# Kernel tuning notes

Hardware: AMD Instinct MI355X
Metric: run time of the kernel (lower is better)

The kernel has to match this reference:

```python
import jax, jax.numpy as jnp
import numpy as np

C_M, C_Z, C_H = 256, 128, 32
S, N = 128, 384
EPS = 1e-5


def setup_inputs() -> dict:
    key = jax.random.key(0)
    ks = jax.random.split(key, 8)
    sc = 1.0 / np.sqrt(C_M)
    return {
        "msa": jax.random.normal(ks[0], (S, N, C_M), dtype=jnp.float32),
        "ln_g": jnp.ones((C_M,), dtype=jnp.float32),
        "ln_b": jnp.zeros((C_M,), dtype=jnp.float32),
        "Wl": jax.random.uniform(ks[1], (C_M, C_H), jnp.float32, -sc, sc),
        "bl": jax.random.uniform(ks[2], (C_H,), jnp.float32, -sc, sc),
        "Wr": jax.random.uniform(ks[3], (C_M, C_H), jnp.float32, -sc, sc),
        "br": jax.random.uniform(ks[4], (C_H,), jnp.float32, -sc, sc),
        "Wo": jax.random.uniform(ks[5], (C_H * C_H, C_Z), jnp.float32, -1.0 / C_H, 1.0 / C_H),
        "bo": jax.random.uniform(ks[6], (C_Z,), jnp.float32, -1.0 / C_H, 1.0 / C_H),
    }


def _layernorm(x, g, b):
    mu = jnp.mean(x, axis=-1, keepdims=True)
    var = jnp.mean(jnp.square(x - mu), axis=-1, keepdims=True)
    return (x - mu) * jax.lax.rsqrt(var + EPS) * g + b


def reference(msa, ln_g, ln_b, Wl, bl, Wr, br, Wo, bo):
    s = msa.shape[0]
    m = _layernorm(msa, ln_g, ln_b)          # [s, n, c_m]
    left = m @ Wl + bl                        # [s, n, c_h]
    right = m @ Wr + br                       # [s, n, c_h]
    outer = jnp.einsum('sic,sjd->ijcd', left, right) / s  # [n, n, c_h, c_h]
    outer = outer.reshape(outer.shape[0], outer.shape[1], -1)
    return outer @ Wo + bo                    # [n, n, c_z]
```

## Files before the change

kernel.cpp:

```cpp
#include <hip/hip_runtime.h>
#include <hip/hip_bf16.h>

#define CM 256
#define CZ 128
#define CH 32
#define SS 128
#define NN 384

typedef short bf16x8 __attribute__((ext_vector_type(8)));
typedef float f32x4 __attribute__((ext_vector_type(4)));
typedef unsigned short us4 __attribute__((ext_vector_type(4)));
typedef unsigned short us8 __attribute__((ext_vector_type(8)));

__device__ __forceinline__ unsigned short f2bf(float f) {
    __hip_bfloat16 h = __float2bfloat16(f);
    return __builtin_bit_cast(unsigned short, h);
}

__global__ __launch_bounds__(256) void k0_transpose(
    const float* __restrict__ Wo, const float* __restrict__ Wl, const float* __restrict__ Wr,
    unsigned short* __restrict__ WoF, unsigned short* __restrict__ WT) {
    int n = blockIdx.x;
    int base = n * 1024;
#pragma unroll
    for (int u = 0; u < 4; u++) {
        int w   = base + u * 256 + threadIdx.x;
        int e   = w & 7;
        int l   = (w >> 3) & 63;
        int zb  = (w >> 9) & 7;
        int cch = w >> 12;
        WoF[w] = f2bf(Wo[(size_t)(cch * 32 + (l >> 4) * 8 + e) * CZ + zb * 16 + (l & 15)]);
    }
    int k = threadIdx.x;
    if (n < 32) {
        WT[n * CM + k] = f2bf(Wl[(size_t)k * CH + n]);
    } else if (n < 64) {
        WT[32 * CM + (n - 32) * CM + k] = f2bf(Wr[(size_t)k * CH + (n - 32)]);
    }
}

__global__ __launch_bounds__(256, 2) void k1_ln_proj(
    const float* __restrict__ msa, const float* __restrict__ g, const float* __restrict__ bta,
    const unsigned short* __restrict__ WT, const float* __restrict__ bl, const float* __restrict__ br,
    unsigned short* __restrict__ Lt, unsigned short* __restrict__ Rt)
{
    __shared__ unsigned short A_lds[64 * 264];
    __shared__ unsigned short B_lds[64 * 264];

    const int i    = blockIdx.x;
    const int sh   = blockIdx.y;
    const int t    = threadIdx.x;
    const int wv   = t >> 6;
    const int lane = t & 63;
    const int lr   = lane & 15, lg = lane >> 4;

    const float4 gv = ((const float4*)g)[lane];
    const float4 bv = ((const float4*)bta)[lane];
#pragma unroll 4
    for (int r = 0; r < 16; r++) {
        int sl = wv * 16 + r;
        int s  = sh * 64 + sl;
        float4 v = ((const float4*)(msa + ((size_t)s * NN + i) * CM))[lane];
        float sum = v.x + v.y + v.z + v.w;
        float sq  = v.x * v.x + v.y * v.y + v.z * v.z + v.w * v.w;
#pragma unroll
        for (int off = 32; off >= 1; off >>= 1) {
            sum += __shfl_xor(sum, off, 64);
            sq  += __shfl_xor(sq, off, 64);
        }
        float mu = sum * (1.f / CM);
        float rs = rsqrtf(sq * (1.f / CM) - mu * mu + 1e-5f);
        us4 pk;
        pk[0] = f2bf((v.x - mu) * rs * gv.x + bv.x);
        pk[1] = f2bf((v.y - mu) * rs * gv.y + bv.y);
        pk[2] = f2bf((v.z - mu) * rs * gv.z + bv.z);
        pk[3] = f2bf((v.w - mu) * rs * gv.w + bv.w);
        *(us4*)&A_lds[sl * 264 + lane * 4] = pk;
    }
#pragma unroll
    for (int u = 0; u < 8; u++) {
        int id = u * 256 + t;
        *(us8*)&B_lds[(id >> 5) * 264 + (id & 31) * 8] = *(const us8*)&WT[id * 8];
    }
    __syncthreads();

    const int m0 = (wv >> 1) * 32;
    const int n0 = (wv & 1) * 32;
    f32x4 acc[2][2];
#pragma unroll
    for (int a = 0; a < 2; a++)
#pragma unroll
        for (int b = 0; b < 2; b++) acc[a][b] = (f32x4){0.f, 0.f, 0.f, 0.f};

#pragma unroll
    for (int ks = 0; ks < 8; ks++) {
        int ko = ks * 32 + lg * 8;
        bf16x8 a0 = *(const bf16x8*)&A_lds[(m0 + lr) * 264 + ko];
        bf16x8 a1 = *(const bf16x8*)&A_lds[(m0 + 16 + lr) * 264 + ko];
        bf16x8 b0 = *(const bf16x8*)&B_lds[(n0 + lr) * 264 + ko];
        bf16x8 b1 = *(const bf16x8*)&B_lds[(n0 + 16 + lr) * 264 + ko];
        acc[0][0] = __builtin_amdgcn_mfma_f32_16x16x32_bf16(a0, b0, acc[0][0], 0, 0, 0);
        acc[0][1] = __builtin_amdgcn_mfma_f32_16x16x32_bf16(a0, b1, acc[0][1], 0, 0, 0);
        acc[1][0] = __builtin_amdgcn_mfma_f32_16x16x32_bf16(a1, b0, acc[1][0], 0, 0, 0);
        acc[1][1] = __builtin_amdgcn_mfma_f32_16x16x32_bf16(a1, b1, acc[1][1], 0, 0, 0);
    }

    const bool isL = (n0 == 0);
    const float scale = isL ? 0.0078125f : 1.f;
#pragma unroll
    for (int mt = 0; mt < 2; mt++)
#pragma unroll
        for (int nt = 0; nt < 2; nt++) {
            int ch = (n0 + nt * 16 + lr) & 31;
            float bias = isL ? bl[ch] : br[ch];
            us4 pk;
#pragma unroll
            for (int rg = 0; rg < 4; rg++)
                pk[rg] = f2bf((acc[mt][nt][rg] + bias) * scale);
            unsigned short* dst = (isL ? Lt : Rt) + (size_t)(i * CH + ch) * SS
                                  + sh * 64 + m0 + mt * 16 + lg * 4;
            *(us4*)dst = pk;
        }
}

#define TI 8
#define TJ 8
#define P1_B_OFF 69632
#define OH1_OFF  65536
#define K2_LDS   139264

__global__ __launch_bounds__(512, 2) void k2_fused(
    const unsigned short* __restrict__ Lt, const unsigned short* __restrict__ Rt,
    const unsigned short* __restrict__ WoF, const float* __restrict__ bo,
    float* __restrict__ out)
{
    extern __shared__ char smem[];
    unsigned short* A = (unsigned short*)(smem);
    unsigned short* B = (unsigned short*)(smem + P1_B_OFF);

    const int i0 = blockIdx.x * TI;
    const int j0 = blockIdx.y * TJ;
    const int t  = threadIdx.x;
    const int wv = t >> 6, lane = t & 63;
    const int lr = lane & 15, lg = lane >> 4;

    const unsigned short* gA = Lt + (size_t)i0 * CH * SS;
    const unsigned short* gB = Rt + (size_t)j0 * CH * SS;
#pragma unroll
    for (int it = 0; it < 8; it++) {
        int c  = it * 512 + t;
        int rw = c >> 4, kc = c & 15;
        *(us8*)(A + rw * 136 + kc * 8) = *(const us8*)(gA + rw * 128 + kc * 8);
        *(us8*)(B + rw * 136 + kc * 8) = *(const us8*)(gB + rw * 128 + kc * 8);
    }
    __syncthreads();

    const int m0  = (wv >> 2) * 128;
    const int n0w = (wv & 3) * 64;

    f32x4 accE[4][4], accO[4][4];
#pragma unroll
    for (int a = 0; a < 4; a++)
#pragma unroll
        for (int b = 0; b < 4; b++) {
            accE[a][b] = (f32x4){0.f, 0.f, 0.f, 0.f};
            accO[a][b] = (f32x4){0.f, 0.f, 0.f, 0.f};
        }

#pragma unroll
    for (int ks = 0; ks < 4; ks++) {
        int ko = ks * 32 + lg * 8;
        bf16x8 af[8], bfr[4];
#pragma unroll
        for (int mt = 0; mt < 8; mt++) af[mt]  = *(const bf16x8*)(A + (m0 + mt * 16 + lr) * 136 + ko);
#pragma unroll
        for (int nt = 0; nt < 4; nt++) bfr[nt] = *(const bf16x8*)(B + (n0w + nt * 16 + lr) * 136 + ko);
#pragma unroll
        for (int mt = 0; mt < 8; mt++)
#pragma unroll
            for (int nt = 0; nt < 4; nt++) {
                if (mt & 1)
                    accO[mt >> 1][nt] = __builtin_amdgcn_mfma_f32_16x16x32_bf16(bfr[nt], af[mt], accO[mt >> 1][nt], 0, 0, 0);
                else
                    accE[mt >> 1][nt] = __builtin_amdgcn_mfma_f32_16x16x32_bf16(bfr[nt], af[mt], accE[mt >> 1][nt], 0, 0, 0);
            }
    }
    __syncthreads();

    const int zsl = wv & 1, ksl = wv >> 1;

    bf16x8 wcur[4], wnxt[4];
#pragma unroll
    for (int bi = 0; bi < 4; bi++)
        wcur[bi] = *(const bf16x8*)&WoF[(((size_t)ksl * 8 + zsl * 4 + bi) * 64 + lane) * 8];

    {
        unsigned short* Oh0 = (unsigned short*)smem;
        unsigned short* Oh1 = (unsigned short*)(smem + OH1_OFF);
#pragma unroll
        for (int mh = 0; mh < 4; mh++) {
            int iiw  = (wv >> 2) * 4 + mh;
            int rowH = iiw * 16 + lr;
            int okey = (rowH ^ (rowH >> 4)) & 7;
#pragma unroll
            for (int nt = 0; nt < 4; nt++) {
                int colBase = n0w + nt * 16 + lg * 4;
                int chk = (colBase >> 3) ^ okey;
                int off = rowH * 256 + chk * 8 + (lg & 1) * 4;
                us4 pkE, pkO;
#pragma unroll
                for (int rg = 0; rg < 4; rg++) {
                    pkE[rg] = f2bf(accE[mh][nt][rg]);
                    pkO[rg] = f2bf(accO[mh][nt][rg]);
                }
                *(us4*)&Oh0[off] = pkE;
                *(us4*)&Oh1[off] = pkO;
            }
        }
    }
    __syncthreads();

    f32x4 acc2[4][4];
#pragma unroll
    for (int a = 0; a < 4; a++)
#pragma unroll
        for (int b = 0; b < 4; b++) acc2[a][b] = (f32x4){0.f, 0.f, 0.f, 0.f};

#pragma unroll
    for (int c = 0; c < 8; c++) {
        if (c < 7) {
            int cchn = (c + 1) * 4 + ksl;
#pragma unroll
            for (int bi = 0; bi < 4; bi++)
                wnxt[bi] = *(const bf16x8*)&WoF[(((size_t)cchn * 8 + zsl * 4 + bi) * 64 + lane) * 8];
        }

        const int cch = c * 4 + ksl;
        const int hh  = cch >> 4;
        const int cH  = cch & 15;
        const unsigned short* OhX = (const unsigned short*)(smem + (hh ? OH1_OFF : 0));

        bf16x8 af2[4];
#pragma unroll
        for (int ai = 0; ai < 4; ai++) {
            int rowH = (ai * 2 + ((lane >> 3) & 1)) * 16 + cH;
            int okey = (rowH ^ (rowH >> 4)) & 7;
            int chk  = (((lane & 7) * 4 + lg) ^ okey);
            af2[ai] = *(const bf16x8*)&OhX[rowH * 256 + chk * 8];
        }
#pragma unroll
        for (int ai = 0; ai < 4; ai++)
#pragma unroll
            for (int bi = 0; bi < 4; bi++)
                acc2[ai][bi] = __builtin_amdgcn_mfma_f32_16x16x32_bf16(af2[ai], wcur[bi], acc2[ai][bi], 0, 0, 0);

        if (c < 7) {
#pragma unroll
            for (int bi = 0; bi < 4; bi++) wcur[bi] = wnxt[bi];
        }
    }
    __syncthreads();

    float* RB = (float*)smem;
#pragma unroll
    for (int ai = 0; ai < 4; ai++)
#pragma unroll
        for (int bi = 0; bi < 4; bi++) {
            int z  = zsl * 64 + bi * 16 + lr;
            int pr = ai * 16 + lg * 4;
            *(f32x4*)&RB[ksl * 8704 + z * 68 + pr] = acc2[ai][bi];
        }
    __syncthreads();

    {
        int z = t >> 2, pq = t & 3;
        float bz = bo[z];
#pragma unroll
        for (int u = 0; u < 4; u++) {
            int p0r = pq * 16 + u * 4;
            f32x4 s = (f32x4){0.f, 0.f, 0.f, 0.f};
#pragma unroll
            for (int ks2 = 0; ks2 < 4; ks2++)
                s += *(const f32x4*)&RB[ks2 * 8704 + z * 68 + p0r];
#pragma unroll
            for (int e = 0; e < 4; e++) {
                int p = p0r + e;
                out[((size_t)(i0 + (p >> 3)) * NN + (j0 + (p & 7))) * CZ + z] = s[e] + bz;
            }
        }
    }
}

extern "C" void kernel_launch(void* const* d_in, const int* in_sizes, int n_in,
                              void* d_out, int out_size, void* d_ws, size_t ws_size,
                              hipStream_t stream) {
    const float* msa  = (const float*)d_in[0];
    const float* ln_g = (const float*)d_in[1];
    const float* ln_b = (const float*)d_in[2];
    const float* Wl   = (const float*)d_in[3];
    const float* bl   = (const float*)d_in[4];
    const float* Wr   = (const float*)d_in[5];
    const float* br   = (const float*)d_in[6];
    const float* Wo   = (const float*)d_in[7];
    const float* bo   = (const float*)d_in[8];
    float* out = (float*)d_out;

    unsigned short* Lt  = (unsigned short*)d_ws;
    unsigned short* Rt  = Lt + (size_t)NN * CH * SS;
    unsigned short* WoF = Rt + (size_t)NN * CH * SS;
    unsigned short* WT  = WoF + (size_t)CZ * CH * CH;

    hipFuncSetAttribute((const void*)k2_fused,
                        hipFuncAttributeMaxDynamicSharedMemorySize, K2_LDS);

    k0_transpose<<<dim3(CZ), dim3(256), 0, stream>>>(Wo, Wl, Wr, WoF, WT);
    k1_ln_proj<<<dim3(NN, 2), dim3(256), 0, stream>>>(msa, ln_g, ln_b, WT, bl, br, Lt, Rt);
    k2_fused<<<dim3(NN / TI, NN / TJ), dim3(512), K2_LDS, stream>>>(Lt, Rt, WoF, bo, out);
}
```

Before: 206.7 us.

## Stage L/R tiles via async global-to-LDS loads with XOR swizzle and prefetch Wo two ahead

Replaces the register-staged copy of the L and R tiles into padded LDS with direct global_load_lds transfers into an XOR-swizzled, unpadded layout. The copy is split into two K halves so the second half loads while MFMAs run on the first. The Wo fragment prefetch becomes a two-deep ring to hide more global latency. The changes add more waitcnt/barrier points and rely on the swizzle keeping LDS reads free of bank conflicts.

```diff
diff --git a/kernel.cpp b/kernel.cpp
--- a/kernel.cpp
+++ b/kernel.cpp
@@ -15,6 +15,13 @@
 __device__ __forceinline__ unsigned short f2bf(float f) {
     __hip_bfloat16 h = __float2bfloat16(f);
     return __builtin_bit_cast(unsigned short, h);
+}
+
+__device__ __forceinline__ void gl_lds16(const unsigned short* g, unsigned short* l) {
+    __builtin_amdgcn_global_load_lds(
+        (const __attribute__((address_space(1))) unsigned int*)g,
+        (__attribute__((address_space(3))) unsigned int*)l,
+        16, 0, 0);
 }
 
 __global__ __launch_bounds__(256) void k0_transpose(
@@ -125,9 +132,12 @@
 
 #define TI 8
 #define TJ 8
-#define P1_B_OFF 69632
+#define P1_B_OFF 65536
 #define OH1_OFF  65536
 #define K2_LDS   139264
+
+#define FRAG(base, row, o) \
+    (*(const bf16x8*)((base) + (((o) & 8) << 11) + (row) * 64 + ((((o) & 7) ^ ((row) & 7)) << 3)))
 
 __global__ __launch_bounds__(512, 2) void k2_fused(
     const unsigned short* __restrict__ Lt, const unsigned short* __restrict__ Rt,
@@ -146,14 +156,24 @@
 
     const unsigned short* gA = Lt + (size_t)i0 * CH * SS;
     const unsigned short* gB = Rt + (size_t)j0 * CH * SS;
-#pragma unroll
-    for (int it = 0; it < 8; it++) {
-        int c  = it * 512 + t;
-        int rw = c >> 4, kc = c & 15;
-        *(us8*)(A + rw * 136 + kc * 8) = *(const us8*)(gA + rw * 128 + kc * 8);
-        *(us8*)(B + rw * 136 + kc * 8) = *(const us8*)(gB + rw * 128 + kc * 8);
-    }
-    __syncthreads();
+
+    auto stage_half = [&](const unsigned short* gS, unsigned short* lS, int h) {
+#pragma unroll
+        for (int p = 0; p < 4; p++) {
+            int q = wv * 4 + p;
+            int d = q * 64 + lane;
+            int row = d >> 3, ow = d & 7;
+            const unsigned short* src = gS + row * 128 + (h * 8 + (ow ^ (row & 7))) * 8;
+            gl_lds16(src, lS + h * 16384 + q * 512);
+        }
+    };
+
+    stage_half(gA, A, 0);
+    stage_half(gB, B, 0);
+    asm volatile("s_waitcnt vmcnt(0)" ::: "memory");
+    __syncthreads();
+    stage_half(gA, A, 1);
+    stage_half(gB, B, 1);
 
     const int m0  = (wv >> 2) * 128;
     const int n0w = (wv & 3) * 64;
@@ -168,13 +188,13 @@
         }
 
 #pragma unroll
-    for (int ks = 0; ks < 4; ks++) {
-        int ko = ks * 32 + lg * 8;
+    for (int ks = 0; ks < 2; ks++) {
+        int o = ks * 4 + lg;
         bf16x8 af[8], bfr[4];
 #pragma unroll
-        for (int mt = 0; mt < 8; mt++) af[mt]  = *(const bf16x8*)(A + (m0 + mt * 16 + lr) * 136 + ko);
-#pragma unroll
-        for (int nt = 0; nt < 4; nt++) bfr[nt] = *(const bf16x8*)(B + (n0w + nt * 16 + lr) * 136 + ko);
+        for (int mt = 0; mt < 8; mt++) af[mt]  = FRAG(A, m0 + mt * 16 + lr, o);
+#pragma unroll
+        for (int nt = 0; nt < 4; nt++) bfr[nt] = FRAG(B, n0w + nt * 16 + lr, o);
 #pragma unroll
         for (int mt = 0; mt < 8; mt++)
 #pragma unroll
@@ -185,14 +205,37 @@
                     accE[mt >> 1][nt] = __builtin_amdgcn_mfma_f32_16x16x32_bf16(bfr[nt], af[mt], accE[mt >> 1][nt], 0, 0, 0);
             }
     }
+    asm volatile("s_waitcnt vmcnt(0)" ::: "memory");
+    __syncthreads();
+#pragma unroll
+    for (int ks = 2; ks < 4; ks++) {
+        int o = ks * 4 + lg;
+        bf16x8 af[8], bfr[4];
+#pragma unroll
+        for (int mt = 0; mt < 8; mt++) af[mt]  = FRAG(A, m0 + mt * 16 + lr, o);
+#pragma unroll
+        for (int nt = 0; nt < 4; nt++) bfr[nt] = FRAG(B, n0w + nt * 16 + lr, o);
+#pragma unroll
+        for (int mt = 0; mt < 8; mt++)
+#pragma unroll
+            for (int nt = 0; nt < 4; nt++) {
+                if (mt & 1)
+                    accO[mt >> 1][nt] = __builtin_amdgcn_mfma_f32_16x16x32_bf16(bfr[nt], af[mt], accO[mt >> 1][nt], 0, 0, 0);
+                else
+                    accE[mt >> 1][nt] = __builtin_amdgcn_mfma_f32_16x16x32_bf16(bfr[nt], af[mt], accE[mt >> 1][nt], 0, 0, 0);
+            }
+    }
     __syncthreads();
 
     const int zsl = wv & 1, ksl = wv >> 1;
 
-    bf16x8 wcur[4], wnxt[4];
+    bf16x8 wbuf[2][4];
 #pragma unroll
     for (int bi = 0; bi < 4; bi++)
-        wcur[bi] = *(const bf16x8*)&WoF[(((size_t)ksl * 8 + zsl * 4 + bi) * 64 + lane) * 8];
+        wbuf[0][bi] = *(const bf16x8*)&WoF[(((size_t)(0 * 4 + ksl) * 8 + zsl * 4 + bi) * 64 + lane) * 8];
+#pragma unroll
+    for (int bi = 0; bi < 4; bi++)
+        wbuf[1][bi] = *(const bf16x8*)&WoF[(((size_t)(1 * 4 + ksl) * 8 + zsl * 4 + bi) * 64 + lane) * 8];
 
     {
         unsigned short* Oh0 = (unsigned short*)smem;
@@ -228,13 +271,6 @@
 
 #pragma unroll
     for (int c = 0; c < 8; c++) {
-        if (c < 7) {
-            int cchn = (c + 1) * 4 + ksl;
-#pragma unroll
-            for (int bi = 0; bi < 4; bi++)
-                wnxt[bi] = *(const bf16x8*)&WoF[(((size_t)cchn * 8 + zsl * 4 + bi) * 64 + lane) * 8];
-        }
-
         const int cch = c * 4 + ksl;
         const int hh  = cch >> 4;
         const int cH  = cch & 15;
@@ -252,11 +288,13 @@
         for (int ai = 0; ai < 4; ai++)
 #pragma unroll
             for (int bi = 0; bi < 4; bi++)
-                acc2[ai][bi] = __builtin_amdgcn_mfma_f32_16x16x32_bf16(af2[ai], wcur[bi], acc2[ai][bi], 0, 0, 0);
-
-        if (c < 7) {
-#pragma unroll
-            for (int bi = 0; bi < 4; bi++) wcur[bi] = wnxt[bi];
+                acc2[ai][bi] = __builtin_amdgcn_mfma_f32_16x16x32_bf16(af2[ai], wbuf[c & 1][bi], acc2[ai][bi], 0, 0, 0);
+
+        if (c < 6) {
+            int cchn = (c + 2) * 4 + ksl;
+#pragma unroll
+            for (int bi = 0; bi < 4; bi++)
+                wbuf[c & 1][bi] = *(const bf16x8*)&WoF[(((size_t)cchn * 8 + zsl * 4 + bi) * 64 + lane) * 8];
         }
     }
     __syncthreads();
```

Measured after the change: 203.1 us. Within noise of the previous version (-1.8%).

## Swizzle k2 phase-1 LDS layout, prefetch Wo two chunks ahead, deepen LN unroll

Applied to the files above, without the earlier changes.

Replaces the padded row stride (136) for the Lt/Rt tiles in LDS with an XOR-swizzled layout split into two K-halves, which removes padding and is meant to avoid bank conflicts on fragment reads. The Wo fragment prefetch becomes double-buffered two chunks ahead, and the first two chunks are issued before the barrier so global latency overlaps the phase-1 to phase-2 transition. The LN loop in k1 is unrolled further. The risks are higher register pressure under the 2-blocks-per-CU launch bound and correctness depending on the new B offset lining up with the swizzled layout.

```diff
diff --git a/kernel.cpp b/kernel.cpp
--- a/kernel.cpp
+++ b/kernel.cpp
@@ -56,7 +56,7 @@
 
     const float4 gv = ((const float4*)g)[lane];
     const float4 bv = ((const float4*)bta)[lane];
-#pragma unroll 4
+#pragma unroll 8
     for (int r = 0; r < 16; r++) {
         int sl = wv * 16 + r;
         int s  = sh * 64 + sl;
@@ -125,9 +125,12 @@
 
 #define TI 8
 #define TJ 8
-#define P1_B_OFF 69632
+#define P1_B_OFF 65536
 #define OH1_OFF  65536
 #define K2_LDS   139264
+
+#define FRAG(base, row, o) \
+    (*(const bf16x8*)((base) + (((o) & 8) << 11) + (row) * 64 + ((((o) & 7) ^ ((row) & 7)) << 3)))
 
 __global__ __launch_bounds__(512, 2) void k2_fused(
     const unsigned short* __restrict__ Lt, const unsigned short* __restrict__ Rt,
@@ -147,11 +150,12 @@
     const unsigned short* gA = Lt + (size_t)i0 * CH * SS;
     const unsigned short* gB = Rt + (size_t)j0 * CH * SS;
 #pragma unroll
-    for (int it = 0; it < 8; it++) {
-        int c  = it * 512 + t;
-        int rw = c >> 4, kc = c & 15;
-        *(us8*)(A + rw * 136 + kc * 8) = *(const us8*)(gA + rw * 128 + kc * 8);
-        *(us8*)(B + rw * 136 + kc * 8) = *(const us8*)(gB + rw * 128 + kc * 8);
+    for (int u = 0; u < 8; u++) {
+        int c   = u * 512 + t;
+        int row = c >> 4, kc = c & 15;
+        int dst = (kc >> 3) * 16384 + row * 64 + ((kc & 7) ^ (row & 7)) * 8;
+        *(us8*)(A + dst) = *(const us8*)(gA + row * 128 + kc * 8);
+        *(us8*)(B + dst) = *(const us8*)(gB + row * 128 + kc * 8);
     }
     __syncthreads();
 
@@ -169,12 +173,12 @@
 
 #pragma unroll
     for (int ks = 0; ks < 4; ks++) {
-        int ko = ks * 32 + lg * 8;
+        int o = ks * 4 + lg;
         bf16x8 af[8], bfr[4];
 #pragma unroll
-        for (int mt = 0; mt < 8; mt++) af[mt]  = *(const bf16x8*)(A + (m0 + mt * 16 + lr) * 136 + ko);
-#pragma unroll
-        for (int nt = 0; nt < 4; nt++) bfr[nt] = *(const bf16x8*)(B + (n0w + nt * 16 + lr) * 136 + ko);
+        for (int mt = 0; mt < 8; mt++) af[mt]  = FRAG(A, m0 + mt * 16 + lr, o);
+#pragma unroll
+        for (int nt = 0; nt < 4; nt++) bfr[nt] = FRAG(B, n0w + nt * 16 + lr, o);
 #pragma unroll
         for (int mt = 0; mt < 8; mt++)
 #pragma unroll
@@ -185,14 +189,18 @@
                     accE[mt >> 1][nt] = __builtin_amdgcn_mfma_f32_16x16x32_bf16(bfr[nt], af[mt], accE[mt >> 1][nt], 0, 0, 0);
             }
     }
-    __syncthreads();
 
     const int zsl = wv & 1, ksl = wv >> 1;
 
-    bf16x8 wcur[4], wnxt[4];
+    bf16x8 wbuf[2][4];
 #pragma unroll
     for (int bi = 0; bi < 4; bi++)
-        wcur[bi] = *(const bf16x8*)&WoF[(((size_t)ksl * 8 + zsl * 4 + bi) * 64 + lane) * 8];
+        wbuf[0][bi] = *(const bf16x8*)&WoF[(((size_t)(0 * 4 + ksl) * 8 + zsl * 4 + bi) * 64 + lane) * 8];
+#pragma unroll
+    for (int bi = 0; bi < 4; bi++)
+        wbuf[1][bi] = *(const bf16x8*)&WoF[(((size_t)(1 * 4 + ksl) * 8 + zsl * 4 + bi) * 64 + lane) * 8];
+
+    __syncthreads();
 
     {
         unsigned short* Oh0 = (unsigned short*)smem;
@@ -228,13 +236,6 @@
 
 #pragma unroll
     for (int c = 0; c < 8; c++) {
-        if (c < 7) {
-            int cchn = (c + 1) * 4 + ksl;
-#pragma unroll
-            for (int bi = 0; bi < 4; bi++)
-                wnxt[bi] = *(const bf16x8*)&WoF[(((size_t)cchn * 8 + zsl * 4 + bi) * 64 + lane) * 8];
-        }
-
         const int cch = c * 4 + ksl;
         const int hh  = cch >> 4;
         const int cH  = cch & 15;
@@ -252,11 +253,13 @@
         for (int ai = 0; ai < 4; ai++)
 #pragma unroll
             for (int bi = 0; bi < 4; bi++)
-                acc2[ai][bi] = __builtin_amdgcn_mfma_f32_16x16x32_bf16(af2[ai], wcur[bi], acc2[ai][bi], 0, 0, 0);
-
-        if (c < 7) {
-#pragma unroll
-            for (int bi = 0; bi < 4; bi++) wcur[bi] = wnxt[bi];
+                acc2[ai][bi] = __builtin_amdgcn_mfma_f32_16x16x32_bf16(af2[ai], wbuf[c & 1][bi], acc2[ai][bi], 0, 0, 0);
+
+        if (c < 6) {
+            int cchn = (c + 2) * 4 + ksl;
+#pragma unroll
+            for (int bi = 0; bi < 4; bi++)
+                wbuf[c & 1][bi] = *(const bf16x8*)&WoF[(((size_t)cchn * 8 + zsl * 4 + bi) * 64 + lane) * 8];
         }
     }
     __syncthreads();
```

Result: no change. 210.1 us (+1.6%).

## Load B operand directly to registers and deepen Wo prefetch in fused kernel

Applied to the files above, without the earlier changes.

In the fused outer-product kernel, the B (right projection) tile is now read from global memory straight into MFMA operand registers instead of being staged through LDS. The A tile is loaded to registers first and then written to LDS, which overlaps the two global loads. The Wo weight prefetch becomes a four-deep register ring issued before the LDS barrier, replacing one-ahead double buffering, and the LN loop unroll is raised. The aim is to cut LDS traffic and hide global load latency, at the cost of many more live registers, which may cause spills or lower occupancy.

```diff
diff --git a/kernel.cpp b/kernel.cpp
--- a/kernel.cpp
+++ b/kernel.cpp
@@ -56,7 +56,7 @@
 
     const float4 gv = ((const float4*)g)[lane];
     const float4 bv = ((const float4*)bta)[lane];
-#pragma unroll 4
+#pragma unroll 8
     for (int r = 0; r < 16; r++) {
         int sl = wv * 16 + r;
         int s  = sh * 64 + sl;
@@ -125,7 +125,6 @@
 
 #define TI 8
 #define TJ 8
-#define P1_B_OFF 69632
 #define OH1_OFF  65536
 #define K2_LDS   139264
 
@@ -136,7 +135,6 @@
 {
     extern __shared__ char smem[];
     unsigned short* A = (unsigned short*)(smem);
-    unsigned short* B = (unsigned short*)(smem + P1_B_OFF);
 
     const int i0 = blockIdx.x * TI;
     const int j0 = blockIdx.y * TJ;
@@ -144,19 +142,30 @@
     const int wv = t >> 6, lane = t & 63;
     const int lr = lane & 15, lg = lane >> 4;
 
+    const int m0  = (wv >> 2) * 128;
+    const int n0w = (wv & 3) * 64;
+
     const unsigned short* gA = Lt + (size_t)i0 * CH * SS;
     const unsigned short* gB = Rt + (size_t)j0 * CH * SS;
-#pragma unroll
-    for (int it = 0; it < 8; it++) {
-        int c  = it * 512 + t;
-        int rw = c >> 4, kc = c & 15;
-        *(us8*)(A + rw * 136 + kc * 8) = *(const us8*)(gA + rw * 128 + kc * 8);
-        *(us8*)(B + rw * 136 + kc * 8) = *(const us8*)(gB + rw * 128 + kc * 8);
-    }
-    __syncthreads();
-
-    const int m0  = (wv >> 2) * 128;
-    const int n0w = (wv & 3) * 64;
+
+    us8 rA[8];
+#pragma unroll
+    for (int u = 0; u < 8; u++) {
+        int c = u * 512 + t;
+        rA[u] = *(const us8*)(gA + (c >> 4) * 128 + (c & 15) * 8);
+    }
+    bf16x8 breg[16];
+#pragma unroll
+    for (int nt = 0; nt < 4; nt++)
+#pragma unroll
+        for (int ks = 0; ks < 4; ks++)
+            breg[nt * 4 + ks] = *(const bf16x8*)(gB + (n0w + nt * 16 + lr) * 128 + (ks * 4 + lg) * 8);
+#pragma unroll
+    for (int u = 0; u < 8; u++) {
+        int c = u * 512 + t;
+        *(us8*)(A + (c >> 4) * 136 + (c & 15) * 8) = rA[u];
+    }
+    __syncthreads();
 
     f32x4 accE[4][4], accO[4][4];
 #pragma unroll
@@ -170,29 +179,29 @@
 #pragma unroll
     for (int ks = 0; ks < 4; ks++) {
         int ko = ks * 32 + lg * 8;
-        bf16x8 af[8], bfr[4];
-#pragma unroll
-        for (int mt = 0; mt < 8; mt++) af[mt]  = *(const bf16x8*)(A + (m0 + mt * 16 + lr) * 136 + ko);
-#pragma unroll
-        for (int nt = 0; nt < 4; nt++) bfr[nt] = *(const bf16x8*)(B + (n0w + nt * 16 + lr) * 136 + ko);
-#pragma unroll
-        for (int mt = 0; mt < 8; mt++)
+#pragma unroll
+        for (int mt = 0; mt < 8; mt++) {
+            bf16x8 af = *(const bf16x8*)&A[(m0 + mt * 16 + lr) * 136 + ko];
 #pragma unroll
             for (int nt = 0; nt < 4; nt++) {
                 if (mt & 1)
-                    accO[mt >> 1][nt] = __builtin_amdgcn_mfma_f32_16x16x32_bf16(bfr[nt], af[mt], accO[mt >> 1][nt], 0, 0, 0);
+                    accO[mt >> 1][nt] = __builtin_amdgcn_mfma_f32_16x16x32_bf16(breg[nt * 4 + ks], af, accO[mt >> 1][nt], 0, 0, 0);
                 else
-                    accE[mt >> 1][nt] = __builtin_amdgcn_mfma_f32_16x16x32_bf16(bfr[nt], af[mt], accE[mt >> 1][nt], 0, 0, 0);
+                    accE[mt >> 1][nt] = __builtin_amdgcn_mfma_f32_16x16x32_bf16(breg[nt * 4 + ks], af, accE[mt >> 1][nt], 0, 0, 0);
             }
-    }
-    __syncthreads();
+        }
+    }
 
     const int zsl = wv & 1, ksl = wv >> 1;
 
-    bf16x8 wcur[4], wnxt[4];
-#pragma unroll
-    for (int bi = 0; bi < 4; bi++)
-        wcur[bi] = *(const bf16x8*)&WoF[(((size_t)ksl * 8 + zsl * 4 + bi) * 64 + lane) * 8];
+    bf16x8 wbuf[4][4];
+#pragma unroll
+    for (int pc = 0; pc < 4; pc++)
+#pragma unroll
+        for (int bi = 0; bi < 4; bi++)
+            wbuf[pc][bi] = *(const bf16x8*)&WoF[(((size_t)(pc * 4 + ksl) * 8 + zsl * 4 + bi) * 64 + lane) * 8];
+
+    __syncthreads();
 
     {
         unsigned short* Oh0 = (unsigned short*)smem;
@@ -228,13 +237,6 @@
 
 #pragma unroll
     for (int c = 0; c < 8; c++) {
-        if (c < 7) {
-            int cchn = (c + 1) * 4 + ksl;
-#pragma unroll
-            for (int bi = 0; bi < 4; bi++)
-                wnxt[bi] = *(const bf16x8*)&WoF[(((size_t)cchn * 8 + zsl * 4 + bi) * 64 + lane) * 8];
-        }
-
         const int cch = c * 4 + ksl;
         const int hh  = cch >> 4;
         const int cH  = cch & 15;
@@ -252,11 +254,13 @@
         for (int ai = 0; ai < 4; ai++)
 #pragma unroll
             for (int bi = 0; bi < 4; bi++)
-                acc2[ai][bi] = __builtin_amdgcn_mfma_f32_16x16x32_bf16(af2[ai], wcur[bi], acc2[ai][bi], 0, 0, 0);
-
-        if (c < 7) {
-#pragma unroll
-            for (int bi = 0; bi < 4; bi++) wcur[bi] = wnxt[bi];
+                acc2[ai][bi] = __builtin_amdgcn_mfma_f32_16x16x32_bf16(af2[ai], wbuf[c & 3][bi], acc2[ai][bi], 0, 0, 0);
+
+        if (c < 4) {
+            int cchn = (c + 4) * 4 + ksl;
+#pragma unroll
+            for (int bi = 0; bi < 4; bi++)
+                wbuf[c & 3][bi] = *(const bf16x8*)&WoF[(((size_t)cchn * 8 + zsl * 4 + bi) * 64 + lane) * 8];
         }
     }
     __syncthreads();
```

After: 229.9 us. +11.2%, slower.
